# Optimization experiments

Hardware: AMD Instinct MI355X
Metric: run time of the kernel (lower is better)

Reference implementation:

```python
import jax, jax.numpy as jnp
import numpy as np

DIM = 1024
GRID_SIZE = 5
SPLINE_ORDER = 3
N_TOKENS = 8192
EPS = 1e-6


def setup_inputs() -> dict:
    key = jax.random.key(0)
    k1, k2, k3 = jax.random.split(key, 3)
    x = jax.random.normal(k1, (N_TOKENS, DIM), dtype=jnp.float32)
    norm_weight = jnp.ones((DIM,), dtype=jnp.float32)
    # nn.Linear default init ~ U(-1/sqrt(dim), 1/sqrt(dim)); randn scaled is fine for a numeric baseline
    base_weight = jax.random.normal(k2, (DIM, DIM), dtype=jnp.float32) * (1.0 / np.sqrt(DIM))
    spline_weight = jax.random.normal(k3, (DIM, GRID_SIZE), dtype=jnp.float32) * 0.1
    gamma = jnp.full((DIM,), 1e-5, dtype=jnp.float32)
    return {"x": x, "norm_weight": norm_weight, "base_weight": base_weight,
            "spline_weight": spline_weight, "gamma": gamma}


def _knots():
    h = 2.0 / GRID_SIZE
    n_knots = GRID_SIZE + SPLINE_ORDER + 1
    return jnp.linspace(-1.0 - SPLINE_ORDER * h, 1.0 + SPLINE_ORDER * h, n_knots)


def _b_spline_basis(x_clamped, knots):
    # x_clamped: (N, D) -> bases: (N, D, grid_size)
    xe = x_clamped[..., None]  # (N, D, 1)
    bases = ((xe >= knots[:-1]) & (xe < knots[1:])).astype(x_clamped.dtype)
    for k in range(1, SPLINE_ORDER + 1):  # fixed small unroll (Cox-de Boor)
        n = bases.shape[-1] - 1
        left_den = jnp.maximum(knots[k:k + n] - knots[:n], 1e-8)
        left = (xe - knots[:n]) / left_den * bases[..., :n]
        right_den = jnp.maximum(knots[k + 1:k + 1 + n] - knots[1:1 + n], 1e-8)
        right = (knots[k + 1:k + 1 + n] - xe) / right_den * bases[..., 1:1 + n]
        bases = left + right
    return bases


def reference(x, norm_weight, base_weight, spline_weight, gamma):
    knots = _knots()
    # RMSNorm
    xf = x.astype(jnp.float32)
    x_norm = (xf * jax.lax.rsqrt(jnp.mean(xf * xf, axis=-1, keepdims=True) + EPS)).astype(x.dtype)
    x_norm = x_norm * norm_weight
    # base path: Linear(dim, dim, bias=False) -> x @ W.T
    base_out = x_norm @ base_weight.T
    # spline path
    x_clamped = jnp.clip(x_norm, -1.0, 1.0)
    spline_bases = _b_spline_basis(x_clamped, knots)  # (N, D, grid_size)
    spline_out = jnp.einsum('ndb,db->nd', spline_bases, spline_weight)
    return x + (base_out + spline_out) * gamma
```

## Files before the change

kernel.cpp:

```cpp
#include <hip/hip_runtime.h>
#include <hip/hip_bf16.h>
#include <stdint.h>

#define DIM 1024
#define NTOK 8192

#define BM 64
#define BN 128
#define BK 64

typedef unsigned char uchar;
typedef __attribute__((ext_vector_type(4)))  int   i32x4;
typedef __attribute__((ext_vector_type(8)))  int   i32x8;
typedef __attribute__((ext_vector_type(4)))  float f32x4;
typedef __attribute__((ext_vector_type(16))) float f32x16;

#define GLOAD_LDS16(g, l)                                                \
    __builtin_amdgcn_global_load_lds(                                    \
        (const __attribute__((address_space(1))) void*)(g),              \
        (__attribute__((address_space(3))) void*)(l), 16, 0, 0)

__device__ __forceinline__ unsigned short f2bf(float f) {
    union { float f; uint32_t u; } v; v.f = f;
    uint32_t u = v.u;
    u += 0x7FFFu + ((u >> 16) & 1u);
    return (unsigned short)(u >> 16);
}
__device__ __forceinline__ float bf2f(unsigned short h) {
    union { uint32_t u; float f; } v; v.u = ((uint32_t)h) << 16; return v.f;
}

__device__ __forceinline__ float spline_eval(float xn, float s0, float s1,
                                             float s2, float s3, float s4) {
    const float xc = fminf(fmaxf(xn, -1.0f), 1.0f);
    const float u = (xc + 2.2f) * (1.0f / 0.55f);
    int j = (int)u;
    j = j < 2 ? 2 : (j > 5 ? 5 : j);
    const float t = u - (float)j;
    const float omt = 1.0f - t;
    const float t2 = t * t, t3 = t2 * t;
    const float w0 = omt * omt * omt * (1.0f / 6.0f);
    const float w1 = (3.0f * t3 - 6.0f * t2 + 4.0f) * (1.0f / 6.0f);
    const float w2 = (-3.0f * t3 + 3.0f * t2 + 3.0f * t + 1.0f) * (1.0f / 6.0f);
    const float w3 = t3 * (1.0f / 6.0f);
    float so;
    if (j == 2)      so = w1 * s0 + w2 * s1 + w3 * s2;
    else if (j == 3) so = w0 * s0 + w1 * s1 + w2 * s2 + w3 * s3;
    else if (j == 4) so = w0 * s1 + w1 * s2 + w2 * s3 + w3 * s4;
    else             so = w0 * s2 + w1 * s3 + w2 * s4;
    return so;
}

__device__ __forceinline__ int pack_fp8x4(float a, float b, float c, float d) {
    int p = __builtin_amdgcn_cvt_pk_fp8_f32(a, b, 0, false);
    p = __builtin_amdgcn_cvt_pk_fp8_f32(c, d, p, true);
    return p;
}

__global__ __launch_bounds__(256) void prep_kernel(
    const float* __restrict__ x, const float* __restrict__ nw,
    const float* __restrict__ W,
    uchar* __restrict__ xn8, uchar* __restrict__ W8,
    float* __restrict__ rr)
{
    const int bid = blockIdx.x;
    const int t = threadIdx.x;
    const int lane = t & 63, w = t >> 6;

    if (bid >= NTOK / 4) {
        const int row = (bid - NTOK / 4) * 4 + w;
        const float4* src = reinterpret_cast<const float4*>(W + (size_t)row * DIM) + lane * 4;
        const float4 a = src[0], b = src[1], c = src[2], d = src[3];
        int4 o;
        o.x = pack_fp8x4(a.x, a.y, a.z, a.w);
        o.y = pack_fp8x4(b.x, b.y, b.z, b.w);
        o.z = pack_fp8x4(c.x, c.y, c.z, c.w);
        o.w = pack_fp8x4(d.x, d.y, d.z, d.w);
        reinterpret_cast<int4*>(W8 + (size_t)row * DIM)[lane] = o;
        return;
    }

    const int row = bid * 4 + w;
    const float4* xr = reinterpret_cast<const float4*>(x + (size_t)row * DIM) + lane * 4;
    const float4 a = xr[0], b = xr[1], c = xr[2], d = xr[3];

    float ssq = a.x*a.x + a.y*a.y + a.z*a.z + a.w*a.w
              + b.x*b.x + b.y*b.y + b.z*b.z + b.w*b.w
              + c.x*c.x + c.y*c.y + c.z*c.z + c.w*c.w
              + d.x*d.x + d.y*d.y + d.z*d.z + d.w*d.w;
    #pragma unroll
    for (int off = 32; off; off >>= 1) ssq += __shfl_xor(ssq, off, 64);

    const float r = rsqrtf(ssq * (1.0f / DIM) + 1e-6f);
    if (lane == 0) rr[row] = r;

    const float4* nwr = reinterpret_cast<const float4*>(nw) + lane * 4;
    const float4 na = nwr[0], nb = nwr[1], nc = nwr[2], nd = nwr[3];
    int4 o;
    o.x = pack_fp8x4(a.x*r*na.x, a.y*r*na.y, a.z*r*na.z, a.w*r*na.w);
    o.y = pack_fp8x4(b.x*r*nb.x, b.y*r*nb.y, b.z*r*nb.z, b.w*r*nb.w);
    o.z = pack_fp8x4(c.x*r*nc.x, c.y*r*nc.y, c.z*r*nc.z, c.w*r*nc.w);
    o.w = pack_fp8x4(d.x*r*nd.x, d.y*r*nd.y, d.z*r*nd.z, d.w*r*nd.w);
    reinterpret_cast<int4*>(xn8 + (size_t)row * DIM)[lane] = o;
}

__global__ __launch_bounds__(256, 3) void gemm_ep_kernel(
    const uchar* __restrict__ A,
    const uchar* __restrict__ B,
    const float* __restrict__ x,
    const float* __restrict__ rrow,
    const float* __restrict__ nw,
    const float* __restrict__ sw,
    const float* __restrict__ gamma,
    float* __restrict__ out)
{
    __shared__ uchar SB[4 * 12288];

    const int tid = threadIdx.x;
    const int lane = tid & 63, wid = tid >> 6;

    const int bid = blockIdx.x;
    const int local = bid >> 3;
    const int bn = local & 7;
    const int bm = (bid & 7) * 16 + (local >> 3);

    const int wm = wid >> 1, wn = wid & 1;

    f32x16 acc[2] = {};

    const int srow = tid >> 2;
    const int scol = ((tid & 3) ^ ((tid >> 3) & 3)) * 16;
    const uchar* Ag = A + (size_t)(bm * BM + srow) * DIM + scol;
    const uchar* Bg = B + (size_t)(bn * BN + srow) * DIM + scol;
    const int oA = tid * 16;
    const int oB = 4096 + tid * 16;

    const int xorv = (lane >> 1) & 3;
    const int u0 = ((lane >> 5) * 2) ^ xorv;
    const int u1 = u0 ^ 1;
    const int aBase = (wm * 32 + (lane & 31)) * 64;
    const int bBase = 4096 + (wn * 64 + (lane & 31)) * 64;

#define STAGE(bi, kt) do {                                           \
        uchar* sb_ = SB + (bi) * 12288;                              \
        const uchar* a_ = Ag + (size_t)(kt) * BK;                    \
        const uchar* b_ = Bg + (size_t)(kt) * BK;                    \
        GLOAD_LDS16(a_,            sb_ + oA);                        \
        GLOAD_LDS16(b_,            sb_ + oB);                        \
        GLOAD_LDS16(b_ + 64 * DIM, sb_ + oB + 4096);                 \
    } while (0)

#define LD8(dst, base) do {                                          \
        const i32x4 lo_ = *reinterpret_cast<const i32x4*>(sb_ + (base) + u0 * 16); \
        const i32x4 hi_ = *reinterpret_cast<const i32x4*>(sb_ + (base) + u1 * 16); \
        dst = (i32x8){lo_[0], lo_[1], lo_[2], lo_[3],                \
                      hi_[0], hi_[1], hi_[2], hi_[3]};               \
    } while (0)

#define COMP(bi) do {                                                \
        const uchar* sb_ = SB + (bi) * 12288;                        \
        i32x8 a0, b0, b1;                                            \
        LD8(a0, aBase);                                              \
        LD8(b0, bBase);                                              \
        LD8(b1, bBase + 2048);                                       \
        acc[0] = __builtin_amdgcn_mfma_scale_f32_32x32x64_f8f6f4(    \
            a0, b0, acc[0], 0, 0, 0, 0x7F7F7F7F, 0, 0x7F7F7F7F);     \
        acc[1] = __builtin_amdgcn_mfma_scale_f32_32x32x64_f8f6f4(    \
            a0, b1, acc[1], 0, 0, 0, 0x7F7F7F7F, 0, 0x7F7F7F7F);     \
    } while (0)

#define W6v asm volatile("s_waitcnt vmcnt(6)" ::: "memory")
#define W3v asm volatile("s_waitcnt vmcnt(3)" ::: "memory")
#define W0v asm volatile("s_waitcnt vmcnt(0)" ::: "memory")
#define BAR __builtin_amdgcn_s_barrier()

    STAGE(0, 0);
    STAGE(1, 1);
    #pragma unroll 1
    for (int k4 = 0; k4 < 12; k4 += 4) {
        STAGE(2, k4 + 2); W6v; BAR; COMP(0);
        STAGE(3, k4 + 3); W6v; BAR; COMP(1);
        STAGE(0, k4 + 4); W6v; BAR; COMP(2);
        STAGE(1, k4 + 5); W6v; BAR; COMP(3);
    }
    STAGE(2, 14); W6v; BAR; COMP(0);
    STAGE(3, 15); W6v; BAR; COMP(1);
    W3v; BAR; COMP(2);
    W0v; BAR; COMP(3);
    __syncthreads();

#undef STAGE
#undef LD8
#undef COMP
#undef W6v
#undef W3v
#undef W0v
#undef BAR

    unsigned short* Cb = reinterpret_cast<unsigned short*>(SB);
    {
        const int crow0 = wm * 32 + 4 * (lane >> 5);
        const int ccol0 = wn * 64 + (lane & 31);
        #pragma unroll
        for (int j = 0; j < 2; ++j)
            #pragma unroll
            for (int r = 0; r < 16; ++r) {
                const int lr = crow0 + (r & 3) + 8 * (r >> 2);
                Cb[lr * 136 + ccol0 + j * 32] = f2bf(acc[j][r]);
            }
    }
    __syncthreads();

    const int colg = bn * BN + (tid & 31) * 4;
    float sf[20];
    {
        const float4* swp = reinterpret_cast<const float4*>(sw + (size_t)colg * 5);
        #pragma unroll
        for (int q = 0; q < 5; ++q) {
            const float4 w4 = swp[q];
            sf[q * 4 + 0] = w4.x; sf[q * 4 + 1] = w4.y;
            sf[q * 4 + 2] = w4.z; sf[q * 4 + 3] = w4.w;
        }
    }
    const float4 gv  = *reinterpret_cast<const float4*>(gamma + colg);
    const float4 nwv = *reinterpret_cast<const float4*>(nw + colg);

    #pragma unroll
    for (int v = 0; v < 8; ++v) {
        const int lr = (tid >> 5) * 8 + v;
        const size_t grow = (size_t)(bm * BM + lr);
        const ushort4 cb4 = *reinterpret_cast<const ushort4*>(&Cb[lr * 136 + (tid & 31) * 4]);
        const float4 xv = *reinterpret_cast<const float4*>(x + grow * DIM + colg);
        const float rv = rrow[grow];
        float4 ov;
        ov.x = xv.x + (bf2f(cb4.x) + spline_eval(xv.x * rv * nwv.x, sf[0],  sf[1],  sf[2],  sf[3],  sf[4]))  * gv.x;
        ov.y = xv.y + (bf2f(cb4.y) + spline_eval(xv.y * rv * nwv.y, sf[5],  sf[6],  sf[7],  sf[8],  sf[9]))  * gv.y;
        ov.z = xv.z + (bf2f(cb4.z) + spline_eval(xv.z * rv * nwv.z, sf[10], sf[11], sf[12], sf[13], sf[14])) * gv.z;
        ov.w = xv.w + (bf2f(cb4.w) + spline_eval(xv.w * rv * nwv.w, sf[15], sf[16], sf[17], sf[18], sf[19])) * gv.w;
        *reinterpret_cast<float4*>(out + grow * DIM + colg) = ov;
    }
}

extern "C" void kernel_launch(void* const* d_in, const int* in_sizes, int n_in,
                              void* d_out, int out_size, void* d_ws, size_t ws_size,
                              hipStream_t stream) {
    const float* x     = (const float*)d_in[0];
    const float* nw    = (const float*)d_in[1];
    const float* W     = (const float*)d_in[2];
    const float* sw    = (const float*)d_in[3];
    const float* gamma = (const float*)d_in[4];
    float* out = (float*)d_out;

    uchar* xn8 = (uchar*)d_ws;
    uchar* W8  = xn8 + (size_t)NTOK * DIM;
    float* rr  = (float*)(W8 + (size_t)DIM * DIM);

    prep_kernel<<<dim3(NTOK / 4 + DIM / 4), 256, 0, stream>>>(x, nw, W, xn8, W8, rr);
    gemm_ep_kernel<<<dim3((NTOK / BM) * (DIM / BN)), 256, 0, stream>>>(
        xn8, W8, x, rr, nw, sw, gamma, out);
}
```

Before: 42.94 us.

## Enlarge GEMM tile to 128x128 with 512-thread blocks

Doubles the M tile of the fp8 GEMM to 128 rows and launches 8 waves per block, so each thread issues one A and one B global-to-LDS load per stage. The stage buffers grow to 16 KB and the vmcnt waits are retuned to match. Block-index swizzling is reworked for the new grid of 512 blocks. The larger tile raises operand reuse per block, at the cost of more LDS per block and fewer blocks in flight. The epilogue, which is not shown, must now handle 128 rows; if it still assumes a 64-row tile, some output rows would go wrong.

```diff
diff --git a/kernel.cpp b/kernel.cpp
--- a/kernel.cpp
+++ b/kernel.cpp
@@ -5,7 +5,7 @@
 #define DIM 1024
 #define NTOK 8192
 
-#define BM 64
+#define BM 128
 #define BN 128
 #define BK 64
 
@@ -104,7 +104,7 @@
     reinterpret_cast<int4*>(xn8 + (size_t)row * DIM)[lane] = o;
 }
 
-__global__ __launch_bounds__(256, 3) void gemm_ep_kernel(
+__global__ __launch_bounds__(512, 4) void gemm_ep_kernel(
     const uchar* __restrict__ A,
     const uchar* __restrict__ B,
     const float* __restrict__ x,
@@ -114,15 +114,14 @@
     const float* __restrict__ gamma,
     float* __restrict__ out)
 {
-    __shared__ uchar SB[4 * 12288];
+    __shared__ uchar SB[4 * 16384];
 
     const int tid = threadIdx.x;
     const int lane = tid & 63, wid = tid >> 6;
 
     const int bid = blockIdx.x;
-    const int local = bid >> 3;
-    const int bn = local & 7;
-    const int bm = (bid & 7) * 16 + (local >> 3);
+    const int swz = (bid & 7) * 64 + (bid >> 3);
+    const int bm = swz >> 3, bn = swz & 7;
 
     const int wm = wid >> 1, wn = wid & 1;
 
@@ -133,21 +132,18 @@
     const uchar* Ag = A + (size_t)(bm * BM + srow) * DIM + scol;
     const uchar* Bg = B + (size_t)(bn * BN + srow) * DIM + scol;
     const int oA = tid * 16;
-    const int oB = 4096 + tid * 16;
+    const int oB = 8192 + tid * 16;
 
     const int xorv = (lane >> 1) & 3;
     const int u0 = ((lane >> 5) * 2) ^ xorv;
     const int u1 = u0 ^ 1;
     const int aBase = (wm * 32 + (lane & 31)) * 64;
-    const int bBase = 4096 + (wn * 64 + (lane & 31)) * 64;
+    const int bBase = 8192 + (wn * 64 + (lane & 31)) * 64;
 
 #define STAGE(bi, kt) do {                                           \
-        uchar* sb_ = SB + (bi) * 12288;                              \
-        const uchar* a_ = Ag + (size_t)(kt) * BK;                    \
-        const uchar* b_ = Bg + (size_t)(kt) * BK;                    \
-        GLOAD_LDS16(a_,            sb_ + oA);                        \
-        GLOAD_LDS16(b_,            sb_ + oB);                        \
-        GLOAD_LDS16(b_ + 64 * DIM, sb_ + oB + 4096);                 \
+        uchar* sb_ = SB + (bi) * 16384;                              \
+        GLOAD_LDS16(Ag + (size_t)(kt) * BK, sb_ + oA);               \
+        GLOAD_LDS16(Bg + (size_t)(kt) * BK, sb_ + oB);               \
     } while (0)
 
 #define LD8(dst, base) do {                                          \
@@ -158,7 +154,7 @@
     } while (0)
 
 #define COMP(bi) do {                                                \
-        const uchar* sb_ = SB + (bi) * 12288;                        \
+        const uchar* sb_ = SB + (bi) * 16384;                        \
         i32x8 a0, b0, b1;                                            \
         LD8(a0, aBase);                                              \
         LD8(b0, bBase);                                              \
@@ -169,8 +165,8 @@
             a0, b1, acc[1], 0, 0, 0, 0x7F7F7F7F, 0, 0x7F7F7F7F);     \
     } while (0)
 
-#define W6v asm volatile("s_waitcnt vmcnt(6)" ::: "memory")
-#define W3v asm volatile("s_waitcnt vmcnt(3)" ::: "memory")
+#define W4v asm volatile("s_waitcnt vmcnt(4)" ::: "memory")
+#define W2v asm volatile("s_waitcnt vmcnt(2)" ::: "memory")
 #define W0v asm volatile("s_waitcnt vmcnt(0)" ::: "memory")
 #define BAR __builtin_amdgcn_s_barrier()
 
@@ -178,22 +174,22 @@
     STAGE(1, 1);
     #pragma unroll 1
     for (int k4 = 0; k4 < 12; k4 += 4) {
-        STAGE(2, k4 + 2); W6v; BAR; COMP(0);
-        STAGE(3, k4 + 3); W6v; BAR; COMP(1);
-        STAGE(0, k4 + 4); W6v; BAR; COMP(2);
-        STAGE(1, k4 + 5); W6v; BAR; COMP(3);
-    }
-    STAGE(2, 14); W6v; BAR; COMP(0);
-    STAGE(3, 15); W6v; BAR; COMP(1);
-    W3v; BAR; COMP(2);
+        STAGE(2, k4 + 2); W4v; BAR; COMP(0);
+        STAGE(3, k4 + 3); W4v; BAR; COMP(1);
+        STAGE(0, k4 + 4); W4v; BAR; COMP(2);
+        STAGE(1, k4 + 5); W4v; BAR; COMP(3);
+    }
+    STAGE(2, 14); W4v; BAR; COMP(0);
+    STAGE(3, 15); W4v; BAR; COMP(1);
+    W2v; BAR; COMP(2);
     W0v; BAR; COMP(3);
     __syncthreads();
 
 #undef STAGE
 #undef LD8
 #undef COMP
-#undef W6v
-#undef W3v
+#undef W4v
+#undef W2v
 #undef W0v
 #undef BAR
 
@@ -256,6 +252,6 @@
     float* rr  = (float*)(W8 + (size_t)DIM * DIM);
 
     prep_kernel<<<dim3(NTOK / 4 + DIM / 4), 256, 0, stream>>>(x, nw, W, xn8, W8, rr);
-    gemm_ep_kernel<<<dim3((NTOK / BM) * (DIM / BN)), 256, 0, stream>>>(
+    gemm_ep_kernel<<<dim3((NTOK / BM) * (DIM / BN)), dim3(512), 0, stream>>>(
         xn8, W8, x, rr, nw, sw, gamma, out);
 }
```

Result: faster. 39.16 us (-8.8%).
